# Performance work log

Hardware: AMD Instinct MI355X
Metric: run time of the kernel (lower is better)

The kernel has to match this reference:

```python
import jax, jax.numpy as jnp
import numpy as np

B, S, P = 16, 1024, 1024
D, H, HD = 128, 8, 16      # embed_dim, num_heads, head_dim (qkv_dim)
MS = 32                    # ms_hidden_dim
E = 524288                 # number of edges
TANH_CLIP = 10.0
TEMP = 1.0
EPS = 1e-9


def setup_inputs() -> dict:
    key = jax.random.key(0)
    ks = jax.random.split(key, 12)
    inv = lambda n: 1.0 / np.sqrt(n)
    return {
        "x1": jax.random.normal(ks[0], (B, S, D), jnp.float32),
        "x2": jax.random.normal(ks[1], (B, P, D), jnp.float32),
        "b_idx": jax.random.randint(ks[2], (E,), 0, B, jnp.int32),
        "s_idx": jax.random.randint(ks[3], (E,), 0, S, jnp.int32),
        "p_idx": jax.random.randint(ks[4], (E,), 0, P, jnp.int32),
        "w": jax.random.uniform(ks[5], (E,), jnp.float32),
        "Wqv1": jax.random.normal(ks[6], (D, 2 * D), jnp.float32) * inv(D),
        "Wkv2": jax.random.normal(ks[7], (D, 2 * D), jnp.float32) * inv(D),
        "Wo1": jax.random.normal(ks[8], (D, D), jnp.float32) * inv(D),
        "Wo2": jax.random.normal(ks[9], (D, D), jnp.float32) * inv(D),
        "msW1": jax.random.normal(ks[10], (H, 2, MS), jnp.float32) * inv(2),
        "msb1": jnp.zeros((H, MS), jnp.float32),
        "msW2": jax.random.normal(ks[11], (H, MS, 1), jnp.float32) * inv(MS),
        "msb2": jnp.zeros((H, 1), jnp.float32),
    }


def _mixed_scores(logits, w, msW1, msb1, msW2, msb2):
    # logits: [E, H], w: [E] -> per-head 2->MS->1 MLP (MatNet MixedScoreFF)
    mixed = jnp.stack([logits, jnp.broadcast_to(w[:, None], logits.shape)], axis=-1)  # [E,H,2]
    hid = jax.nn.relu(jnp.einsum('ehi,him->ehm', mixed, msW1) + msb1)  # [E,H,MS]
    out = (jnp.einsum('ehm,hmo->eho', hid, msW2) + msb2)[..., 0]       # [E,H]
    return TANH_CLIP * jnp.tanh(out) / TEMP


def _group_softmax_combine(logits, values, gid, num_groups):
    # logits: [E,H], values: [E,H,HD]; exp -> segment-sum denom -> weighted scatter
    el = jnp.exp(logits)
    denom = jax.ops.segment_sum(el, gid, num_segments=num_groups)      # [G,H]
    attn = el / (denom[gid] + EPS)                                      # [E,H]
    return jax.ops.segment_sum(attn[:, :, None] * values, gid, num_segments=num_groups)  # [G,H,HD]


def reference(x1, x2, b_idx, s_idx, p_idx, w, Wqv1, Wkv2, Wo1, Wo2, msW1, msb1, msW2, msb2):
    qv1 = (x1 @ Wqv1).reshape(B, S, 2, H, HD)   # [B,S,2,H,HD]
    kv2 = (x2 @ Wkv2).reshape(B, P, 2, H, HD)
    row_flat = b_idx * S + s_idx                # [E]
    col_flat = b_idx * P + p_idx
    qv1_e = qv1.reshape(B * S, 2, H, HD)[row_flat]   # [E,2,H,HD]
    kv2_e = kv2.reshape(B * P, 2, H, HD)[col_flat]
    q, v1 = qv1_e[:, 0], qv1_e[:, 1]
    k, v2 = kv2_e[:, 0], kv2_e[:, 1]
    logits = jnp.einsum('ehd,ehd->eh', q, k) / np.sqrt(HD).astype(np.float32)
    logits = _mixed_scores(logits, w, msW1, msb1, msW2, msb2)
    row_heads = _group_softmax_combine(logits, v2, row_flat, B * S)  # [B*S,H,HD]
    col_heads = _group_softmax_combine(logits, v1, col_flat, B * P)  # [B*P,H,HD]
    h1 = row_heads.reshape(B, S, H * HD) @ Wo1
    h2 = col_heads.reshape(B, P, H * HD) @ Wo2
    return h1, h2
```

## Files before the change

kernel.cpp:

```cpp
#include <hip/hip_runtime.h>
#include <hip/hip_fp16.h>
#include <math.h>

#define BB   16
#define SS   1024
#define PP   1024
#define HH   8
#define MSS  32
#define EE   524288
#define NROW (BB*SS)
#define NCOL (BB*PP)
#define ESTRIDE 5
#define NBPX 2112
#define NB   128
#define CHUNK 4096

__device__ __forceinline__ void gemm_tile_core(
        const float* __restrict__ Arow, const float* __restrict__ Bsrc,
        int ldb, int c0, float* As , float* Bs ,
        float4 acc4[8], int t) {
    int tx = t & 31, ty = t >> 5;
#pragma unroll
    for (int li = 0; li < 8; li++) {
        int idx = li * 256 + t;
        int r = idx >> 5, p = idx & 31;
        *(float4*)&As[r * 132 + 4 * p] = *(const float4*)(Arow + r * 128 + 4 * p);
    }
#pragma unroll
    for (int i = 0; i < 8; i++) acc4[i] = make_float4(0.f, 0.f, 0.f, 0.f);

    for (int kc = 0; kc < 4; kc++) {
        __syncthreads();
#pragma unroll
        for (int li = 0; li < 4; li++) {
            int idx = li * 256 + t;
            int kk = idx >> 5, p = idx & 31;
            *(float4*)&Bs[kk * 128 + 4 * p] =
                *(const float4*)(Bsrc + (size_t)(kc * 32 + kk) * ldb + c0 + 4 * p);
        }
        __syncthreads();
#pragma unroll
        for (int kq = 0; kq < 8; kq++) {
            float4 a4[8];
#pragma unroll
            for (int i = 0; i < 8; i++)
                a4[i] = *(const float4*)&As[(ty + 8 * i) * 132 + kc * 32 + kq * 4];
#pragma unroll
            for (int kk = 0; kk < 4; kk++) {
                float4 b4 = *(const float4*)&Bs[(kq * 4 + kk) * 128 + 4 * tx];
#pragma unroll
                for (int i = 0; i < 8; i++) {
                    float av = ((const float*)&a4[i])[kk];
                    acc4[i].x = fmaf(av, b4.x, acc4[i].x);
                    acc4[i].y = fmaf(av, b4.y, acc4[i].y);
                    acc4[i].z = fmaf(av, b4.z, acc4[i].z);
                    acc4[i].w = fmaf(av, b4.w, acc4[i].w);
                }
            }
        }
    }
}

__global__ __launch_bounds__(256) void proj_kernel(
        const float* __restrict__ x1, const float* __restrict__ x2,
        const float* __restrict__ Wqv1, const float* __restrict__ Wkv2,
        float* __restrict__ qf, float* __restrict__ kf,
        __half* __restrict__ v1h, __half* __restrict__ v2h) {
    __shared__ float As[64 * 132];
    __shared__ float Bs[32 * 128];
    int t = threadIdx.x;
    int bid = blockIdx.x;
    int matrix = bid >> 9;
    int ct = (bid >> 8) & 1;
    int mb = bid & 255;
    const float* A  = matrix ? x2 : x1;
    const float* Bm = matrix ? Wkv2 : Wqv1;

    float4 acc4[8];
    gemm_tile_core(A + (size_t)mb * 64 * 128, Bm, 256, ct * 128, As, Bs, acc4, t);

    int tx = t & 31, ty = t >> 5;
    if (ct == 0) {
        float* Cq = matrix ? kf : qf;
#pragma unroll
        for (int i = 0; i < 8; i++) {
            int row = mb * 64 + ty + 8 * i;
            *(float4*)(Cq + (size_t)row * 128 + 4 * tx) = acc4[i];
        }
    } else {
        __half* Cv = matrix ? v2h : v1h;
#pragma unroll
        for (int i = 0; i < 8; i++) {
            int row = mb * 64 + ty + 8 * i;
            __half2* p = (__half2*)(Cv + (size_t)row * 128 + 4 * tx);
            p[0] = __halves2half2(__float2half(acc4[i].x), __float2half(acc4[i].y));
            p[1] = __halves2half2(__float2half(acc4[i].z), __float2half(acc4[i].w));
        }
    }
}

__global__ __launch_bounds__(256) void outp_kernel(
        const float* __restrict__ rh, const float* __restrict__ ch,
        const float* __restrict__ Wo1, const float* __restrict__ Wo2,
        float* __restrict__ out) {
    __shared__ float As[64 * 132];
    __shared__ float Bs[32 * 128];
    int t = threadIdx.x;
    int matrix = blockIdx.x >> 8;
    int mb = blockIdx.x & 255;
    const float* A  = matrix ? ch : rh;
    const float* Bm = matrix ? Wo2 : Wo1;
    float* C = out + (size_t)matrix * NROW * 128;

    float4 acc4[8];
    gemm_tile_core(A + (size_t)mb * 64 * 128, Bm, 128, 0, As, Bs, acc4, t);

    int tx = t & 31, ty = t >> 5;
#pragma unroll
    for (int i = 0; i < 8; i++) {
        int row = mb * 64 + ty + 8 * i;
        *(float4*)(C + (size_t)row * 128 + 4 * tx) = acc4[i];
    }
}

__global__ __launch_bounds__(1024) void hist_kernel(
        const int* __restrict__ b_idx, const int* __restrict__ s_idx,
        const int* __restrict__ p_idx, unsigned int* __restrict__ ph) {
    __shared__ unsigned int lh[16384];
    int t = threadIdx.x;
#pragma unroll
    for (int i = 0; i < 16; i++) lh[t + 1024 * i] = 0;
    __syncthreads();
    int base = blockIdx.x * CHUNK;
#pragma unroll
    for (int k = 0; k < 4; k++) {
        int e = base + k * 1024 + t;
        int b = b_idx[e];
        int rbin = (b << 10) + s_idx[e];
        int cbin = 16384 + (b << 10) + p_idx[e];
        atomicAdd(&lh[rbin >> 1], 1u << (16 * (rbin & 1)));
        atomicAdd(&lh[cbin >> 1], 1u << (16 * (cbin & 1)));
    }
    __syncthreads();
    unsigned int* dst = ph + (size_t)blockIdx.x * 16384;
#pragma unroll
    for (int i = 0; i < 16; i++) dst[t + 1024 * i] = lh[t + 1024 * i];
}

__global__ __launch_bounds__(128) void scan1_kernel(
        const unsigned int* __restrict__ ph, int* __restrict__ pbase,
        int* __restrict__ tot) {
    int bin = blockIdx.x * 128 + threadIdx.x;
    int word = bin >> 1;
    int sh = 16 * (bin & 1);
    int run = 0;
#pragma unroll 8
    for (int j = 0; j < NB; j++) {
        unsigned int v = ph[(size_t)j * 16384 + word];
        pbase[(size_t)j * 32768 + bin] = run;
        run += (v >> sh) & 0xffff;
    }
    tot[bin] = run;
}

__global__ __launch_bounds__(1024) void scan2_kernel(
        const int* __restrict__ tot, int* __restrict__ offs) {
    __shared__ int sdata[1024];
    int side = blockIdx.x;
    int t = threadIdx.x;
    const int* c = tot + side * 16384;
    int* o = offs + side * (16384 + 1);
    int base = t * 16;
    int loc[16];
    int run = 0;
#pragma unroll
    for (int i = 0; i < 16; i++) { loc[i] = run; run += c[base + i]; }
    sdata[t] = run;
    __syncthreads();
    for (int st = 1; st < 1024; st <<= 1) {
        int v = (t >= st) ? sdata[t - st] : 0;
        __syncthreads();
        sdata[t] += v;
        __syncthreads();
    }
    int excl = sdata[t] - run;
#pragma unroll
    for (int i = 0; i < 16; i++) o[base + i] = excl + loc[i];
    if (t == 1023) o[16384] = sdata[1023];
}

__global__ __launch_bounds__(1024) void posc_kernel(
        const int* __restrict__ b_idx, const int* __restrict__ p_idx,
        const int* __restrict__ pbase, const int* __restrict__ offs,
        int* __restrict__ pc_of_e) {
    __shared__ int cur[16384];
    int t = threadIdx.x;
    const int* src = pbase + (size_t)blockIdx.x * 32768 + 16384;
    const int* oc = offs + (16384 + 1);
#pragma unroll
    for (int i = 0; i < 16; i++) {
        int idx = t + 1024 * i;
        cur[idx] = oc[idx] + src[idx];
    }
    __syncthreads();
    int base = blockIdx.x * CHUNK;
#pragma unroll
    for (int k = 0; k < 4; k++) {
        int e = base + k * 1024 + t;
        int cbin = (b_idx[e] << 10) + p_idx[e];
        pc_of_e[e] = atomicAdd(&cur[cbin], 1);
    }
}

__global__ __launch_bounds__(1024) void posr_kernel(
        const int* __restrict__ b_idx, const int* __restrict__ s_idx,
        const int* __restrict__ p_idx, const float* __restrict__ w,
        const int* __restrict__ pbase, const int* __restrict__ offs,
        const int* __restrict__ pc_of_e, int4* __restrict__ ebuf) {
    __shared__ int cur[16384];
    int t = threadIdx.x;
    const int* src = pbase + (size_t)blockIdx.x * 32768;
#pragma unroll
    for (int i = 0; i < 16; i++) {
        int idx = t + 1024 * i;
        cur[idx] = offs[idx] + src[idx];
    }
    __syncthreads();
    int base = blockIdx.x * CHUNK;
#pragma unroll
    for (int k = 0; k < 4; k++) {
        int e = base + k * 1024 + t;
        int b = b_idx[e];
        int row = (b << 10) + s_idx[e];
        int col = (b << 10) + p_idx[e];
        int pr = atomicAdd(&cur[row], 1);
        ebuf[pr] = make_int4(row, col, __float_as_int(w[e]), pc_of_e[e]);
    }
}

__global__ __launch_bounds__(256) void edge_kernel(
        const float* __restrict__ qf, const float* __restrict__ kf,
        const int4* __restrict__ ebuf, const int* __restrict__ offs_row,
        const float* __restrict__ msW1, const float* __restrict__ msb1,
        const float* __restrict__ msW2, const float* __restrict__ msb2,
        float* __restrict__ entr, float* __restrict__ entc) {
    __shared__ float4 sPk[8 * 33];
    __shared__ float sB2[8];
    int t = threadIdx.x;
    {
        int h = t >> 5, m = t & 31;
        sPk[h * 33 + m] = make_float4(msW1[h * 64 + m], msW1[h * 64 + 32 + m],
                                      msb1[h * 32 + m], msW2[h * 32 + m]);
    }
    if (t < 8) sB2[t] = msb2[t];
    __syncthreads();

    int x = blockIdx.x & 7;
    int r0 = blockIdx.x >> 3;
    int a0 = offs_row[x << 10],       a1 = offs_row[(x + 1) << 10];
    int b0 = offs_row[(x + 8) << 10], b1 = offs_row[(x + 9) << 10];
    int nA = a1 - a0;
    int n = nA + (b1 - b0);

    int l = t & 7;
    int sub = t >> 3;
    int hh = 2 * (l & 3) + (l >> 2);
    const float4* wp = &sPk[hh * 33];
    float bias2 = sB2[hh];

    for (int jb = r0 * 32; jb < n; jb += NBPX * 32) {
        int j = jb + sub;
        if (j < n) {
            int pos = (j < nA) ? (a0 + j) : (b0 + (j - nA));
            int4 rec = ebuf[pos];
            int row = rec.x, col = rec.y;
            float we = __int_as_float(rec.z);
            int pc = rec.w;

            const float4* qp4 = (const float4*)(qf + (size_t)row * 128);
            const float4* kp4 = (const float4*)(kf + (size_t)col * 128);
            float p0, p1, p2, p3;
            {
                float4 a = qp4[l],      k4 = kp4[l];
                p0 = fmaf(a.x, k4.x, fmaf(a.y, k4.y, fmaf(a.z, k4.z, a.w * k4.w)));
            }
            {
                float4 a = qp4[8 + l],  k4 = kp4[8 + l];
                p1 = fmaf(a.x, k4.x, fmaf(a.y, k4.y, fmaf(a.z, k4.z, a.w * k4.w)));
            }
            {
                float4 a = qp4[16 + l], k4 = kp4[16 + l];
                p2 = fmaf(a.x, k4.x, fmaf(a.y, k4.y, fmaf(a.z, k4.z, a.w * k4.w)));
            }
            {
                float4 a = qp4[24 + l], k4 = kp4[24 + l];
                p3 = fmaf(a.x, k4.x, fmaf(a.y, k4.y, fmaf(a.z, k4.z, a.w * k4.w)));
            }
            p0 += __shfl_xor(p0, 1); p0 += __shfl_xor(p0, 2);
            p1 += __shfl_xor(p1, 1); p1 += __shfl_xor(p1, 2);
            p2 += __shfl_xor(p2, 1); p2 += __shfl_xor(p2, 2);
            p3 += __shfl_xor(p3, 1); p3 += __shfl_xor(p3, 2);

            int js = l & 3;
            float dot = js == 0 ? p0 : (js == 1 ? p1 : (js == 2 ? p2 : p3));
            float logit = dot * 0.25f;

            float outv = bias2;
#pragma unroll 4
            for (int m = 0; m < MSS; m++) {
                float4 c = wp[m];
                float hid = fmaf(logit, c.x, fmaf(we, c.y, c.z));
                hid = fmaxf(hid, 0.f);
                outv = fmaf(hid, c.w, outv);
            }
            float ev = expf(10.0f * tanhf(outv));
            __half evh = __float2half(ev);

            float* er = entr + (size_t)pos * ESTRIDE;
            float* ec = entc + (size_t)pc * ESTRIDE;
            ((__half*)er)[2 + hh] = evh;
            ((__half*)ec)[2 + hh] = evh;
            if (l == 0) {
                er[0] = __int_as_float(col);
                ec[0] = __int_as_float(row);
            }
        }
    }
}

__global__ __launch_bounds__(128) void combine_kernel(
        const float* __restrict__ entr, const float* __restrict__ entc,
        const int* __restrict__ offs_row, const int* __restrict__ offs_col,
        const __half* __restrict__ v1h, const __half* __restrict__ v2h,
        float* __restrict__ row_heads, float* __restrict__ col_heads) {
    int x = blockIdx.x & 7;
    int r = blockIdx.x >> 3;
    int which = r >> 10;
    int sidx = r & 1023;
    int b = x + ((which & 1) << 3);
    int gl = (b << 10) + sidx;

    int t = threadIdx.x;
    int h = t >> 4;
    const float* ent; const __half* vals; const int* offs; float* outp;
    if (which < 2) { ent = entr; vals = v2h; offs = offs_row; outp = row_heads; }
    else           { ent = entc; vals = v1h; offs = offs_col; outp = col_heads; }
    int s = offs[gl], e_ = offs[gl + 1];
    float acc = 0.f, den = 0.f;
#pragma unroll 4
    for (int i = s; i < e_; i++) {
        const float* en = ent + (size_t)i * ESTRIDE;
        int other = __float_as_int(en[0]);
        float ev = __half2float(((const __half*)en)[2 + h]);
        float v = __half2float(vals[(size_t)other * 128 + t]);
        acc = fmaf(ev, v, acc);
        den += ev;
    }
    outp[(size_t)gl * 128 + t] = acc / (den + 1e-9f);
}

extern "C" void kernel_launch(void* const* d_in, const int* in_sizes, int n_in,
                              void* d_out, int out_size, void* d_ws, size_t ws_size,
                              hipStream_t stream) {
    const float* x1   = (const float*)d_in[0];
    const float* x2   = (const float*)d_in[1];
    const int* b_idx  = (const int*)d_in[2];
    const int* s_idx  = (const int*)d_in[3];
    const int* p_idx  = (const int*)d_in[4];
    const float* w    = (const float*)d_in[5];
    const float* Wqv1 = (const float*)d_in[6];
    const float* Wkv2 = (const float*)d_in[7];
    const float* Wo1  = (const float*)d_in[8];
    const float* Wo2  = (const float*)d_in[9];
    const float* msW1 = (const float*)d_in[10];
    const float* msb1 = (const float*)d_in[11];
    const float* msW2 = (const float*)d_in[12];
    const float* msb2 = (const float*)d_in[13];
    float* out = (float*)d_out;

    float* qf = (float*)d_ws;
    float* kf = qf + (size_t)NROW * 128;
    __half* v1h = (__half*)(kf + (size_t)NCOL * 128);
    __half* v2h = v1h + (size_t)NROW * 128;
    float* entr = (float*)(v2h + (size_t)NCOL * 128);
    float* entc = entr + (size_t)EE * ESTRIDE;
    float* row_heads = entc + (size_t)EE * ESTRIDE;
    float* col_heads = row_heads + (size_t)NROW * 128;
    int4* ebuf = (int4*)(col_heads + (size_t)NCOL * 128);
    int* offs = (int*)(ebuf + EE);
    int* tot  = offs + 2 * (16384 + 1);
    unsigned int* ph = (unsigned int*)entc;
    int* pbase = (int*)row_heads;
    int* pc_of_e = (int*)entr;

    hist_kernel<<<NB, 1024, 0, stream>>>(b_idx, s_idx, p_idx, ph);
    scan1_kernel<<<256, 128, 0, stream>>>(ph, pbase, tot);
    scan2_kernel<<<2, 1024, 0, stream>>>(tot, offs);
    posc_kernel<<<NB, 1024, 0, stream>>>(b_idx, p_idx, pbase, offs, pc_of_e);
    posr_kernel<<<NB, 1024, 0, stream>>>(b_idx, s_idx, p_idx, w, pbase, offs,
                                         pc_of_e, ebuf);

    proj_kernel<<<1024, 256, 0, stream>>>(x1, x2, Wqv1, Wkv2, qf, kf, v1h, v2h);

    edge_kernel<<<8 * NBPX, 256, 0, stream>>>(
        qf, kf, ebuf, offs, msW1, msb1, msW2, msb2, entr, entc);

    combine_kernel<<<2 * NROW, 128, 0, stream>>>(
        entr, entc, offs, offs + (16384 + 1), v1h, v2h, row_heads, col_heads);

    outp_kernel<<<512, 256, 0, stream>>>(row_heads, col_heads, Wo1, Wo2, out);
}
```

Before: 264.2 us.

## Fuse column/row position kernels and stage combine edge entries in LDS

Merges posc and posr into one pos_kernel that computes column positions, then reloads the shared cursor table with row offsets and computes row positions. This drops one launch and the global pc_of_e round trip. The combine kernel now cooperatively copies up to 96 edge entries of a group into shared memory before the accumulation loop, replacing scattered per-thread global reads of the same entry. It adds a block sync and extra shared-memory traffic per group.

```diff
diff --git a/kernel.cpp b/kernel.cpp
--- a/kernel.cpp
+++ b/kernel.cpp
@@ -14,6 +14,7 @@
 #define NBPX 2112
 #define NB   128
 #define CHUNK 4096
+#define GCAP 96
 
 __device__ __forceinline__ void gemm_tile_core(
         const float* __restrict__ Arow, const float* __restrict__ Bsrc,
@@ -189,52 +190,49 @@
     if (t == 1023) o[16384] = sdata[1023];
 }
 
-__global__ __launch_bounds__(1024) void posc_kernel(
-        const int* __restrict__ b_idx, const int* __restrict__ p_idx,
-        const int* __restrict__ pbase, const int* __restrict__ offs,
-        int* __restrict__ pc_of_e) {
-    __shared__ int cur[16384];
-    int t = threadIdx.x;
-    const int* src = pbase + (size_t)blockIdx.x * 32768 + 16384;
-    const int* oc = offs + (16384 + 1);
-#pragma unroll
-    for (int i = 0; i < 16; i++) {
-        int idx = t + 1024 * i;
-        cur[idx] = oc[idx] + src[idx];
-    }
-    __syncthreads();
-    int base = blockIdx.x * CHUNK;
-#pragma unroll
-    for (int k = 0; k < 4; k++) {
-        int e = base + k * 1024 + t;
-        int cbin = (b_idx[e] << 10) + p_idx[e];
-        pc_of_e[e] = atomicAdd(&cur[cbin], 1);
-    }
-}
-
-__global__ __launch_bounds__(1024) void posr_kernel(
+__global__ __launch_bounds__(1024) void pos_kernel(
         const int* __restrict__ b_idx, const int* __restrict__ s_idx,
         const int* __restrict__ p_idx, const float* __restrict__ w,
         const int* __restrict__ pbase, const int* __restrict__ offs,
-        const int* __restrict__ pc_of_e, int4* __restrict__ ebuf) {
+        int4* __restrict__ ebuf) {
     __shared__ int cur[16384];
     int t = threadIdx.x;
-    const int* src = pbase + (size_t)blockIdx.x * 32768;
-#pragma unroll
-    for (int i = 0; i < 16; i++) {
-        int idx = t + 1024 * i;
-        cur[idx] = offs[idx] + src[idx];
+    {
+        const int* src = pbase + (size_t)blockIdx.x * 32768 + 16384;
+        const int* oc = offs + (16384 + 1);
+#pragma unroll
+        for (int i = 0; i < 16; i++) {
+            int idx = t + 1024 * i;
+            cur[idx] = oc[idx] + src[idx];
+        }
     }
     __syncthreads();
     int base = blockIdx.x * CHUNK;
+    int rowr[4], colr[4], pcr[4];
+    float wr[4];
 #pragma unroll
     for (int k = 0; k < 4; k++) {
         int e = base + k * 1024 + t;
         int b = b_idx[e];
-        int row = (b << 10) + s_idx[e];
-        int col = (b << 10) + p_idx[e];
-        int pr = atomicAdd(&cur[row], 1);
-        ebuf[pr] = make_int4(row, col, __float_as_int(w[e]), pc_of_e[e]);
+        rowr[k] = (b << 10) + s_idx[e];
+        colr[k] = (b << 10) + p_idx[e];
+        wr[k] = w[e];
+        pcr[k] = atomicAdd(&cur[colr[k]], 1);
+    }
+    __syncthreads();
+    {
+        const int* src = pbase + (size_t)blockIdx.x * 32768;
+#pragma unroll
+        for (int i = 0; i < 16; i++) {
+            int idx = t + 1024 * i;
+            cur[idx] = offs[idx] + src[idx];
+        }
+    }
+    __syncthreads();
+#pragma unroll
+    for (int k = 0; k < 4; k++) {
+        int pr = atomicAdd(&cur[rowr[k]], 1);
+        ebuf[pr] = make_int4(rowr[k], colr[k], __float_as_int(wr[k]), pcr[k]);
     }
 }
 
@@ -333,6 +331,7 @@
         const int* __restrict__ offs_row, const int* __restrict__ offs_col,
         const __half* __restrict__ v1h, const __half* __restrict__ v2h,
         float* __restrict__ row_heads, float* __restrict__ col_heads) {
+    __shared__ float sE[GCAP * ESTRIDE];
     int x = blockIdx.x & 7;
     int r = blockIdx.x >> 3;
     int which = r >> 10;
@@ -346,10 +345,25 @@
     if (which < 2) { ent = entr; vals = v2h; offs = offs_row; outp = row_heads; }
     else           { ent = entc; vals = v1h; offs = offs_col; outp = col_heads; }
     int s = offs[gl], e_ = offs[gl + 1];
+    int cnt = e_ - s;
+    int cap = cnt < GCAP ? cnt : GCAP;
+
+    const float* gsrc = ent + (size_t)s * ESTRIDE;
+    for (int i = t; i < cap * ESTRIDE; i += 128) sE[i] = gsrc[i];
+    __syncthreads();
+
     float acc = 0.f, den = 0.f;
-#pragma unroll 4
-    for (int i = s; i < e_; i++) {
-        const float* en = ent + (size_t)i * ESTRIDE;
+#pragma unroll 8
+    for (int i = 0; i < cap; i++) {
+        const float* en = &sE[i * ESTRIDE];
+        int other = __float_as_int(en[0]);
+        float ev = __half2float(((const __half*)en)[2 + h]);
+        float v = __half2float(vals[(size_t)other * 128 + t]);
+        acc = fmaf(ev, v, acc);
+        den += ev;
+    }
+    for (int i = cap; i < cnt; i++) {
+        const float* en = gsrc + (size_t)i * ESTRIDE;
         int other = __float_as_int(en[0]);
         float ev = __half2float(((const __half*)en)[2 + h]);
         float v = __half2float(vals[(size_t)other * 128 + t]);
@@ -391,14 +405,11 @@
     int* tot  = offs + 2 * (16384 + 1);
     unsigned int* ph = (unsigned int*)entc;
     int* pbase = (int*)row_heads;
-    int* pc_of_e = (int*)entr;
 
     hist_kernel<<<NB, 1024, 0, stream>>>(b_idx, s_idx, p_idx, ph);
     scan1_kernel<<<256, 128, 0, stream>>>(ph, pbase, tot);
     scan2_kernel<<<2, 1024, 0, stream>>>(tot, offs);
-    posc_kernel<<<NB, 1024, 0, stream>>>(b_idx, p_idx, pbase, offs, pc_of_e);
-    posr_kernel<<<NB, 1024, 0, stream>>>(b_idx, s_idx, p_idx, w, pbase, offs,
-                                         pc_of_e, ebuf);
+    pos_kernel<<<NB, 1024, 0, stream>>>(b_idx, s_idx, p_idx, w, pbase, offs, ebuf);
 
     proj_kernel<<<1024, 256, 0, stream>>>(x1, x2, Wqv1, Wkv2, qf, kf, v1h, v2h);
 
```

New measurement: 244.6 us. -7.4%, faster.
